# Kernel optimization log

Measured on AMD Instinct MI355X. Metric: run time of the kernel, lower is better.

The kernel has to match this reference:

```python
import jax, jax.numpy as jnp
import numpy as np

INPUT_DIM, HID, LAT, FUT = 32, 128, 64, 128
B, T = 1024, 512


def _linear(x, W, b):
    return x @ W.T + b


def _lstm_layer(xs, Wih, Whh, b):
    # xs: [T, B, D_in] -> ys: [T, B, HID], h_T: [B, HID]
    Bsz = xs.shape[1]
    h0 = jnp.zeros((Bsz, HID), xs.dtype)
    c0 = jnp.zeros((Bsz, HID), xs.dtype)

    def step(carry, xt):
        h, c = carry
        g = xt @ Wih.T + h @ Whh.T + b  # [B, 4*HID]
        i, f, gg, o = jnp.split(g, 4, axis=-1)  # torch gate order i,f,g,o
        i = jax.nn.sigmoid(i)
        f = jax.nn.sigmoid(f)
        gg = jnp.tanh(gg)
        o = jax.nn.sigmoid(o)
        c = f * c + i * gg
        h = o * jnp.tanh(c)
        return (h, c), h

    (hT, _), ys = jax.lax.scan(step, (h0, c0), xs)
    return ys, hT


def setup_inputs() -> dict:
    key = jax.random.key(0)
    ks = iter(jax.random.split(key, 40))

    def w(shape, scale=0.05):
        return (jax.random.normal(next(ks), shape, dtype=jnp.float32) * scale)

    inp = {
        "x": jax.random.normal(next(ks), (B, T, INPUT_DIM), dtype=jnp.float32),
        "eps": jax.random.normal(next(ks), (B, LAT), dtype=jnp.float32),
        "u": jax.random.uniform(next(ks), (B, LAT), dtype=jnp.float32, minval=1e-4, maxval=1 - 1e-4),
        "choice": jax.random.uniform(next(ks), (B,), dtype=jnp.float32),
        # 3-layer LSTM params (torch: W_ih [4H, D], W_hh [4H, H], fused bias)
        "Wih0": w((4 * HID, INPUT_DIM)), "Whh0": w((4 * HID, HID)), "b0": w((4 * HID,)),
        "Wih1": w((4 * HID, HID)), "Whh1": w((4 * HID, HID)), "b1": w((4 * HID,)),
        "Wih2": w((4 * HID, HID)), "Whh2": w((4 * HID, HID)), "b2": w((4 * HID,)),
        "ln_g": jnp.ones((HID,), jnp.float32), "ln_b": jnp.zeros((HID,), jnp.float32),
        "fc1_W": w((128, HID)), "fc1_b": w((128,)),
        "fc2_W": w((64, 128)), "fc2_b": w((64,)),
        "mean_W": w((LAT, 64)), "mean_b": w((LAT,)),
        "logvar_W": w((LAT, 64)), "logvar_b": w((LAT,)),
        "scale_W": w((LAT, 64)), "scale_b": w((LAT,)),
        "shape_W": w((LAT, 64)), "shape_b": w((LAT,)),
        "dec1_W": w((128, LAT)), "dec1_b": w((128,)),
        "dec2_W": w((500, 128)), "dec2_b": w((500,)),
        "out_W": w((FUT, 500)), "out_b": w((FUT,)),
        "pi_params": jnp.array([3.0, 0.01], jnp.float32),
    }
    return inp


def reference(x, eps, u, choice,
              Wih0, Whh0, b0, Wih1, Whh1, b1, Wih2, Whh2, b2,
              ln_g, ln_b, fc1_W, fc1_b, fc2_W, fc2_b,
              mean_W, mean_b, logvar_W, logvar_b,
              scale_W, scale_b, shape_W, shape_b,
              dec1_W, dec1_b, dec2_W, dec2_b, out_W, out_b, pi_params):
    # --- Encoder ---
    xs = jnp.transpose(x, (1, 0, 2))  # [T, B, D]
    ys, _ = _lstm_layer(xs, Wih0, Whh0, b0)
    ys, _ = _lstm_layer(ys, Wih1, Whh1, b1)
    _, h = _lstm_layer(ys, Wih2, Whh2, b2)  # final hidden of last layer [B, HID]
    mu = h.mean(-1, keepdims=True)
    var = jnp.mean((h - mu) ** 2, -1, keepdims=True)
    h = (h - mu) * jax.lax.rsqrt(var + 1e-5) * ln_g + ln_b
    hid = jax.nn.relu(_linear(h, fc1_W, fc1_b))
    hid = jax.nn.relu(_linear(hid, fc2_W, fc2_b))  # dropout = identity (eval)
    z_mean = _linear(hid, mean_W, mean_b)
    z_logvar = _linear(hid, logvar_W, logvar_b)
    z_scale = jnp.exp(_linear(hid, scale_W, scale_b))
    z_shape = jnp.maximum(_linear(hid, shape_W, shape_b), 1e-6)
    # --- Reparameterize (vectorized mixture select) ---
    z_gauss = z_mean + eps * jnp.exp(0.5 * z_logvar)
    z_gpd = z_scale / z_shape * ((1.0 - u) ** (-z_shape) - 1.0)
    pi = jax.nn.softmax(pi_params)
    z = jnp.where((choice < pi[0])[:, None], z_gauss, z_gpd)
    # --- Decoder ---
    d = jax.nn.relu(_linear(z, dec1_W, dec1_b))
    d = jax.nn.relu(_linear(d, dec2_W, dec2_b))  # dropout = identity (eval)
    rec = _linear(d, out_W, out_b)
    return rec, z_mean, z_logvar, z_scale, z_shape
```

## Files before the change

### kernel.cpp

```cpp
#include <hip/hip_runtime.h>
#include <math.h>

typedef __attribute__((ext_vector_type(8))) short s16x8;
typedef __attribute__((ext_vector_type(4))) float f32x4;

__device__ __forceinline__ unsigned short f2bf(float f) {
  unsigned int x = __builtin_bit_cast(unsigned int, f);
  x += 0x7fffu + ((x >> 16) & 1u);
  return (unsigned short)(x >> 16);
}
__device__ __forceinline__ float fexp2(float x) { return __builtin_amdgcn_exp2f(x); }
__device__ __forceinline__ float frcp(float x)  { return __builtin_amdgcn_rcpf(x); }
__device__ __forceinline__ float sigm(float x)  { return frcp(1.0f + fexp2(x * -1.4426950408889634f)); }
__device__ __forceinline__ float tanh_fast(float x) {
  return 1.0f - 2.0f * frcp(1.0f + fexp2(x * 2.8853900817779268f));
}

#define MFMA16(A, B, C) __builtin_amdgcn_mfma_f32_16x16x32_bf16((A), (B), (C), 0, 0, 0)

constexpr int TT = 512;
constexpr int NB = 1024;
constexpr int CHUNK = 8;

template <int DIN, bool FIRST, bool LAST>
__device__ __forceinline__ void scan_layer(
    unsigned short* a_lds,
    const float* __restrict__ xin,
    unsigned short* ys,
    const float* __restrict__ Wih,
    const float* __restrict__ Whh,
    const float* __restrict__ bias,
    float* __restrict__ hT,
    int* prog_in, int* prog_out, int bblk)
{
  constexpr int KT = DIN / 32 + 4;
  constexpr int KS = (DIN == 32) ? 192 : 256;

  const int tid = threadIdx.x;
  const int wv = tid >> 6, ln = tid & 63, l15 = ln & 15, lg = ln >> 4;
  const int row0 = bblk * 16;

  s16x8 bfr[4][KT];
#pragma unroll
  for (int j = 0; j < 4; ++j) {
    const int n = j * 128 + wv * 16 + l15;
#pragma unroll
    for (int kt = 0; kt < KT; ++kt) {
      s16x8 f;
#pragma unroll
      for (int e = 0; e < 8; ++e) {
        const int k = kt * 32 + lg * 8 + e;
        const float w = (k < DIN) ? Wih[n * DIN + k] : Whh[n * 128 + (k - DIN)];
        f[e] = (short)f2bf(w);
      }
      bfr[j][kt] = f;
    }
  }
  f32x4 bj[4];
#pragma unroll
  for (int j = 0; j < 4; ++j)
    bj[j] = *reinterpret_cast<const f32x4*>(bias + j * 128 + wv * 16 + lg * 4);

  for (int i = tid; i < 2 * 16 * KS; i += 512) a_lds[i] = 0;
  __syncthreads();

  const int prow = tid >> 5, pcol = tid & 31;
  float xr_f = 0.f;
  unsigned long long xr_h = 0ull;
  int avail = 0;

  if (FIRST) {
    xr_f = xin[(size_t)(row0 + prow) * (TT * 32) + pcol];
    a_lds[(prow * KS + pcol) ^ ((prow & 7) << 3)] = f2bf(xr_f);
  } else {
    int ch;
    do { ch = __hip_atomic_load(prog_in, __ATOMIC_RELAXED, __HIP_MEMORY_SCOPE_AGENT); } while (ch * CHUNK < 1);
    avail = ch * CHUNK;
    asm volatile("" ::: "memory");
    xr_h = __hip_atomic_load(
        (unsigned long long*)ys + ((size_t)(row0 + prow) * 128 + pcol * 4) / 4,
        __ATOMIC_RELAXED, __HIP_MEMORY_SCOPE_AGENT);
    *reinterpret_cast<unsigned long long*>(
        &a_lds[(prow * KS + pcol * 4) ^ ((prow & 7) << 3)]) = xr_h;
  }

  float cst[4] = {0.f, 0.f, 0.f, 0.f};
  const int hcol = wv * 16 + lg * 4;

  for (int t = 0; t < TT; ++t) {
    unsigned short* buf  = a_lds + (t & 1) * (16 * KS);
    unsigned short* nbuf = a_lds + ((t + 1) & 1) * (16 * KS);
    __syncthreads();

    s16x8 afr[KT];
#pragma unroll
    for (int kt = 0; kt < KT; ++kt) {
      const int idx = l15 * KS + kt * 32 + lg * 8;
      afr[kt] = *reinterpret_cast<const s16x8*>(&buf[idx ^ ((l15 & 7) << 3)]);
    }
    f32x4 acc[4];
#pragma unroll
    for (int j = 0; j < 4; ++j) acc[j] = bj[j];
#pragma unroll
    for (int kt = 0; kt < KT; ++kt)
#pragma unroll
      for (int j = 0; j < 4; ++j) acc[j] = MFMA16(bfr[j][kt], afr[kt], acc[j]);

    if (t + 1 < TT) {
      if (FIRST) {
        xr_f = xin[(size_t)(row0 + prow) * (TT * 32) + (t + 1) * 32 + pcol];
      } else {
        if (avail < t + 2) {
          int ch;
          do { ch = __hip_atomic_load(prog_in, __ATOMIC_RELAXED, __HIP_MEMORY_SCOPE_AGENT); } while (ch * CHUNK < t + 2);
          avail = ch * CHUNK;
          asm volatile("" ::: "memory");
        }
        xr_h = __hip_atomic_load(
            (unsigned long long*)ys + ((size_t)(t + 1) * (NB * 128) + (size_t)(row0 + prow) * 128 + pcol * 4) / 4,
            __ATOMIC_RELAXED, __HIP_MEMORY_SCOPE_AGENT);
      }
    }

    float hv[4];
#pragma unroll
    for (int r = 0; r < 4; ++r) {
      const float iv = sigm(acc[0][r]);
      const float fv = sigm(acc[1][r]);
      const float gv = tanh_fast(acc[2][r]);
      const float ov = sigm(acc[3][r]);
      const float cn = fv * cst[r] + iv * gv;
      cst[r] = cn;
      hv[r] = ov * tanh_fast(cn);
    }
    const unsigned int plo = (unsigned int)f2bf(hv[0]) | ((unsigned int)f2bf(hv[1]) << 16);
    const unsigned int phi = (unsigned int)f2bf(hv[2]) | ((unsigned int)f2bf(hv[3]) << 16);
    const unsigned long long hpack = (unsigned long long)plo | ((unsigned long long)phi << 32);

    *reinterpret_cast<unsigned long long*>(
        &nbuf[(l15 * KS + DIN + hcol) ^ ((l15 & 7) << 3)]) = hpack;
    if (t + 1 < TT) {
      if (FIRST) {
        nbuf[(prow * KS + pcol) ^ ((prow & 7) << 3)] = f2bf(xr_f);
      } else {
        *reinterpret_cast<unsigned long long*>(
            &nbuf[(prow * KS + pcol * 4) ^ ((prow & 7) << 3)]) = xr_h;
      }
    }

    if (!LAST) {
      __hip_atomic_store(
          (unsigned long long*)ys + ((size_t)t * (NB * 128) + (size_t)(row0 + l15) * 128 + hcol) / 4,
          hpack, __ATOMIC_RELAXED, __HIP_MEMORY_SCOPE_AGENT);
      if (((t + 1) & (CHUNK - 1)) == 0) {
        asm volatile("s_waitcnt vmcnt(0)" ::: "memory");
        __syncthreads();
        if (tid == 0)
          __hip_atomic_store(prog_out, (t + 1) / CHUNK, __ATOMIC_RELAXED, __HIP_MEMORY_SCOPE_AGENT);
      }
    } else if (t == TT - 1) {
      f32x4 o = {hv[0], hv[1], hv[2], hv[3]};
      *reinterpret_cast<f32x4*>(&hT[(row0 + l15) * 128 + hcol]) = o;
    }
  }
}

__global__ __launch_bounds__(512, 2) void lstm_fused(
    const float* __restrict__ x, unsigned short* ys,
    const float* __restrict__ Wih0, const float* __restrict__ Whh0, const float* __restrict__ b0,
    const float* __restrict__ Wih1, const float* __restrict__ Whh1, const float* __restrict__ b1,
    const float* __restrict__ Wih2, const float* __restrict__ Whh2, const float* __restrict__ b2,
    float* __restrict__ hT, int* prog)
{
  __shared__ unsigned short a_lds[2 * 16 * 256];
  const int lay = blockIdx.x >> 6;
  const int bblk = blockIdx.x & 63;
  if (lay == 0) {
    scan_layer<32, true, false>(a_lds, x, ys, Wih0, Whh0, b0, nullptr,
                                nullptr, &prog[(0 * 64 + bblk) * 4], bblk);
  } else if (lay == 1) {
    scan_layer<128, false, false>(a_lds, nullptr, ys, Wih1, Whh1, b1, nullptr,
                                  &prog[(0 * 64 + bblk) * 4], &prog[(1 * 64 + bblk) * 4], bblk);
  } else {
    scan_layer<128, false, true>(a_lds, nullptr, ys, Wih2, Whh2, b2, hT,
                                 &prog[(1 * 64 + bblk) * 4], nullptr, bblk);
  }
}

__global__ void init_flags(int* prog) { prog[threadIdx.x] = 0; }

__global__ __launch_bounds__(256) void head_kernel(
    const float* __restrict__ hT, const float* __restrict__ eps,
    const float* __restrict__ u, const float* __restrict__ choice,
    const float* __restrict__ ln_g, const float* __restrict__ ln_b,
    const float* __restrict__ fc1_W, const float* __restrict__ fc1_b,
    const float* __restrict__ fc2_W, const float* __restrict__ fc2_b,
    const float* __restrict__ mean_W, const float* __restrict__ mean_b,
    const float* __restrict__ logvar_W, const float* __restrict__ logvar_b,
    const float* __restrict__ scale_W, const float* __restrict__ scale_b,
    const float* __restrict__ shape_W, const float* __restrict__ shape_b,
    const float* __restrict__ dec1_W, const float* __restrict__ dec1_b,
    const float* __restrict__ dec2_W, const float* __restrict__ dec2_b,
    const float* __restrict__ out_W, const float* __restrict__ out_b,
    const float* __restrict__ pi_params, float* __restrict__ out)
{
  __shared__ float s_hn[4][128];
  __shared__ float s_a[4][128];
  __shared__ float s_b2[4][64];
  __shared__ float s_z[4][64];
  __shared__ float s_d1[4][128];
  __shared__ float s_d2[4][512];

  const int tid = threadIdx.x;
  const int gr0 = blockIdx.x * 4;

  {
    const int wvr = tid >> 6, lnn = tid & 63;
    const float v0 = hT[(gr0 + wvr) * 128 + lnn];
    const float v1 = hT[(gr0 + wvr) * 128 + 64 + lnn];
    float s = v0 + v1, s2 = v0 * v0 + v1 * v1;
#pragma unroll
    for (int off = 32; off; off >>= 1) {
      s  += __shfl_xor(s, off, 64);
      s2 += __shfl_xor(s2, off, 64);
    }
    const float mu  = s * (1.f / 128.f);
    const float var = s2 * (1.f / 128.f) - mu * mu;
    const float rs  = rsqrtf(var + 1e-5f);
    s_hn[wvr][lnn]      = (v0 - mu) * rs * ln_g[lnn]      + ln_b[lnn];
    s_hn[wvr][lnn + 64] = (v1 - mu) * rs * ln_g[lnn + 64] + ln_b[lnn + 64];
  }
  __syncthreads();
#pragma unroll
  for (int p = 0; p < 2; ++p) {
    const int idx = tid + p * 256, row = idx >> 7, col = idx & 127;
    const float* w = fc1_W + col * 128;
    float a = fc1_b[col];
    for (int k = 0; k < 128; k += 4)
      a += s_hn[row][k] * w[k] + s_hn[row][k + 1] * w[k + 1] +
           s_hn[row][k + 2] * w[k + 2] + s_hn[row][k + 3] * w[k + 3];
    s_a[row][col] = fmaxf(a, 0.f);
  }
  __syncthreads();
  {
    const int row = tid >> 6, col = tid & 63;
    const float* w = fc2_W + col * 128;
    float a = fc2_b[col];
    for (int k = 0; k < 128; ++k) a += s_a[row][k] * w[k];
    s_b2[row][col] = fmaxf(a, 0.f);
  }
  __syncthreads();
  {
    const int row = tid >> 6, c = tid & 63;
    const int gr = gr0 + row;
    float am = mean_b[c], al = logvar_b[c], as_ = scale_b[c], ah = shape_b[c];
    for (int k = 0; k < 64; ++k) {
      const float hv = s_b2[row][k];
      am  += hv * mean_W[c * 64 + k];
      al  += hv * logvar_W[c * 64 + k];
      as_ += hv * scale_W[c * 64 + k];
      ah  += hv * shape_W[c * 64 + k];
    }
    const float zsc = fexp2(as_ * 1.4426950408889634f);
    const float zsh = fmaxf(ah, 1e-6f);
    out[131072 + gr * 64 + c] = am;
    out[196608 + gr * 64 + c] = al;
    out[262144 + gr * 64 + c] = zsc;
    out[327680 + gr * 64 + c] = zsh;
    const float ev = eps[gr * 64 + c], uv = u[gr * 64 + c], cv = choice[gr];
    const float zg = am + ev * fexp2(0.72134752044448170f * al);
    const float p0 = pi_params[0], p1 = pi_params[1];
    const float pi0 = 1.f / (1.f + expf(p1 - p0));
    const float tq = -zsh * logf(1.f - uv);
    const float zp = zsc * frcp(zsh) * expm1f(tq);
    s_z[row][c] = (cv < pi0) ? zg : zp;
  }
  __syncthreads();
#pragma unroll
  for (int p = 0; p < 2; ++p) {
    const int idx = tid + p * 256, row = idx >> 7, col = idx & 127;
    const float* w = dec1_W + col * 64;
    float a = dec1_b[col];
    for (int k = 0; k < 64; ++k) a += s_z[row][k] * w[k];
    s_d1[row][col] = fmaxf(a, 0.f);
  }
  __syncthreads();
  for (int o = tid; o < 2000; o += 256) {
    const int row = o / 500, col = o % 500;
    const float* w = dec2_W + col * 128;
    float a = dec2_b[col];
    for (int k = 0; k < 128; ++k) a += s_d1[row][k] * w[k];
    s_d2[row][col] = fmaxf(a, 0.f);
  }
  __syncthreads();
#pragma unroll
  for (int p = 0; p < 2; ++p) {
    const int idx = tid + p * 256, row = idx >> 7, col = idx & 127;
    const float* w = out_W + col * 500;
    float a = out_b[col];
    for (int k = 0; k < 500; ++k) a += s_d2[row][k] * w[k];
    out[(gr0 + row) * 128 + col] = a;
  }
}

extern "C" void kernel_launch(void* const* d_in, const int* in_sizes, int n_in,
                              void* d_out, int out_size, void* d_ws, size_t ws_size,
                              hipStream_t stream) {
  const float* x      = (const float*)d_in[0];
  const float* eps    = (const float*)d_in[1];
  const float* u      = (const float*)d_in[2];
  const float* choice = (const float*)d_in[3];
  const float* Wih0 = (const float*)d_in[4],  *Whh0 = (const float*)d_in[5],  *b0 = (const float*)d_in[6];
  const float* Wih1 = (const float*)d_in[7],  *Whh1 = (const float*)d_in[8],  *b1 = (const float*)d_in[9];
  const float* Wih2 = (const float*)d_in[10], *Whh2 = (const float*)d_in[11], *b2 = (const float*)d_in[12];
  const float* ln_g = (const float*)d_in[13], *ln_b = (const float*)d_in[14];
  const float* fc1_W = (const float*)d_in[15], *fc1_b = (const float*)d_in[16];
  const float* fc2_W = (const float*)d_in[17], *fc2_b = (const float*)d_in[18];
  const float* mean_W = (const float*)d_in[19], *mean_b = (const float*)d_in[20];
  const float* logvar_W = (const float*)d_in[21], *logvar_b = (const float*)d_in[22];
  const float* scale_W = (const float*)d_in[23], *scale_b = (const float*)d_in[24];
  const float* shape_W = (const float*)d_in[25], *shape_b = (const float*)d_in[26];
  const float* dec1_W = (const float*)d_in[27], *dec1_b = (const float*)d_in[28];
  const float* dec2_W = (const float*)d_in[29], *dec2_b = (const float*)d_in[30];
  const float* out_W = (const float*)d_in[31], *out_b = (const float*)d_in[32];
  const float* pi_params = (const float*)d_in[33];

  unsigned short* ys = (unsigned short*)d_ws;
  float* hT  = (float*)((char*)d_ws + (size_t)512 * 1024 * 128 * 2);
  int*   prog = (int*)((char*)d_ws + (size_t)512 * 1024 * 128 * 2 + (size_t)1024 * 128 * 4);

  init_flags<<<1, 512, 0, stream>>>(prog);
  lstm_fused<<<192, 512, 0, stream>>>(x, ys, Wih0, Whh0, b0, Wih1, Whh1, b1,
                                      Wih2, Whh2, b2, hT, prog);
  head_kernel<<<256, 256, 0, stream>>>(hT, eps, u, choice, ln_g, ln_b,
      fc1_W, fc1_b, fc2_W, fc2_b, mean_W, mean_b, logvar_W, logvar_b,
      scale_W, scale_b, shape_W, shape_b, dec1_W, dec1_b, dec2_W, dec2_b,
      out_W, out_b, pi_params, (float*)d_out);
}
```

Before: 687.8 us.

## Split input projection from recurrence and batch two timesteps per sync

```diff
diff --git a/kernel.cpp b/kernel.cpp
--- a/kernel.cpp
+++ b/kernel.cpp
@@ -3,6 +3,9 @@
 
 typedef __attribute__((ext_vector_type(8))) short s16x8;
 typedef __attribute__((ext_vector_type(4))) float f32x4;
+typedef unsigned long long ull;
+
+constexpr float LOG2E = 1.4426950408889634f;
 
 __device__ __forceinline__ unsigned short f2bf(float f) {
   unsigned int x = __builtin_bit_cast(unsigned int, f);
@@ -11,156 +14,180 @@
 }
 __device__ __forceinline__ float fexp2(float x) { return __builtin_amdgcn_exp2f(x); }
 __device__ __forceinline__ float frcp(float x)  { return __builtin_amdgcn_rcpf(x); }
-__device__ __forceinline__ float sigm(float x)  { return frcp(1.0f + fexp2(x * -1.4426950408889634f)); }
-__device__ __forceinline__ float tanh_fast(float x) {
-  return 1.0f - 2.0f * frcp(1.0f + fexp2(x * 2.8853900817779268f));
-}
-
-#define MFMA16(A, B, C) __builtin_amdgcn_mfma_f32_16x16x32_bf16((A), (B), (C), 0, 0, 0)
+
+#define MFMA16(A, B, Cc) __builtin_amdgcn_mfma_f32_16x16x32_bf16((A), (B), (Cc), 0, 0, 0)
 
 constexpr int TT = 512;
 constexpr int NB = 1024;
-constexpr int CHUNK = 8;
+constexpr int CH  = 2;
+constexpr int PUB = 4;
 
 template <int DIN, bool FIRST, bool LAST>
 __device__ __forceinline__ void scan_layer(
-    unsigned short* a_lds,
+    unsigned short* x_s,
+    unsigned short* h_s,
+    float* b_s,
     const float* __restrict__ xin,
     unsigned short* ys,
-    const float* __restrict__ Wih,
-    const float* __restrict__ Whh,
-    const float* __restrict__ bias,
-    float* __restrict__ hT,
+    const float* __restrict__ Wih, const float* __restrict__ Whh,
+    const float* __restrict__ bias, float* __restrict__ hT,
     int* prog_in, int* prog_out, int bblk)
 {
-  constexpr int KT = DIN / 32 + 4;
-  constexpr int KS = (DIN == 32) ? 192 : 256;
-
+  constexpr int KTX = DIN / 32;
+  constexpr int XM  = (DIN == 32) ? 3 : 7;
   const int tid = threadIdx.x;
   const int wv = tid >> 6, ln = tid & 63, l15 = ln & 15, lg = ln >> 4;
   const int row0 = bblk * 16;
-
-  s16x8 bfr[4][KT];
+  const int prow = tid >> 5, pcol = tid & 31;
+
+  s16x8 bfx[4][KTX], bfh[4][4];
 #pragma unroll
   for (int j = 0; j < 4; ++j) {
+    const float sc = (j == 2) ? (2.0f * LOG2E) : (-LOG2E);
     const int n = j * 128 + wv * 16 + l15;
 #pragma unroll
-    for (int kt = 0; kt < KT; ++kt) {
+    for (int kt = 0; kt < KTX; ++kt) {
       s16x8 f;
 #pragma unroll
-      for (int e = 0; e < 8; ++e) {
-        const int k = kt * 32 + lg * 8 + e;
-        const float w = (k < DIN) ? Wih[n * DIN + k] : Whh[n * 128 + (k - DIN)];
-        f[e] = (short)f2bf(w);
-      }
-      bfr[j][kt] = f;
-    }
-  }
-  f32x4 bj[4];
-#pragma unroll
-  for (int j = 0; j < 4; ++j)
-    bj[j] = *reinterpret_cast<const f32x4*>(bias + j * 128 + wv * 16 + lg * 4);
-
-  for (int i = tid; i < 2 * 16 * KS; i += 512) a_lds[i] = 0;
-  __syncthreads();
-
-  const int prow = tid >> 5, pcol = tid & 31;
-  float xr_f = 0.f;
-  unsigned long long xr_h = 0ull;
+      for (int e = 0; e < 8; ++e) f[e] = (short)f2bf(Wih[n * DIN + kt * 32 + lg * 8 + e] * sc);
+      bfx[j][kt] = f;
+    }
+#pragma unroll
+    for (int kt = 0; kt < 4; ++kt) {
+      s16x8 f;
+#pragma unroll
+      for (int e = 0; e < 8; ++e) f[e] = (short)f2bf(Whh[n * 128 + kt * 32 + lg * 8 + e] * sc);
+      bfh[j][kt] = f;
+    }
+  }
+  b_s[tid] = bias[tid] * ((tid >> 7) == 2 ? 2.0f * LOG2E : -LOG2E);
+  for (int i = tid; i < 2 * 16 * 128; i += 512) h_s[i] = 0;
+
+  float xrf[CH];
+  ull xrh[CH];
   int avail = 0;
-
   if (FIRST) {
-    xr_f = xin[(size_t)(row0 + prow) * (TT * 32) + pcol];
-    a_lds[(prow * KS + pcol) ^ ((prow & 7) << 3)] = f2bf(xr_f);
+#pragma unroll
+    for (int s = 0; s < CH; ++s)
+      xrf[s] = xin[(size_t)(row0 + prow) * (TT * 32) + s * 32 + pcol];
   } else {
     int ch;
-    do { ch = __hip_atomic_load(prog_in, __ATOMIC_RELAXED, __HIP_MEMORY_SCOPE_AGENT); } while (ch * CHUNK < 1);
-    avail = ch * CHUNK;
-    asm volatile("" ::: "memory");
-    xr_h = __hip_atomic_load(
-        (unsigned long long*)ys + ((size_t)(row0 + prow) * 128 + pcol * 4) / 4,
-        __ATOMIC_RELAXED, __HIP_MEMORY_SCOPE_AGENT);
-    *reinterpret_cast<unsigned long long*>(
-        &a_lds[(prow * KS + pcol * 4) ^ ((prow & 7) << 3)]) = xr_h;
-  }
+    do { ch = __hip_atomic_load(prog_in, __ATOMIC_RELAXED, __HIP_MEMORY_SCOPE_AGENT); } while (ch * PUB < CH);
+    avail = ch * PUB;
+#pragma unroll
+    for (int s = 0; s < CH; ++s)
+      xrh[s] = __hip_atomic_load(
+          (ull*)ys + ((size_t)s * (NB * 128) + (size_t)(row0 + prow) * 128 + pcol * 4) / 4,
+          __ATOMIC_RELAXED, __HIP_MEMORY_SCOPE_AGENT);
+  }
+  __syncthreads();
 
   float cst[4] = {0.f, 0.f, 0.f, 0.f};
   const int hcol = wv * 16 + lg * 4;
 
-  for (int t = 0; t < TT; ++t) {
-    unsigned short* buf  = a_lds + (t & 1) * (16 * KS);
-    unsigned short* nbuf = a_lds + ((t + 1) & 1) * (16 * KS);
+  for (int t0 = 0; t0 < TT; t0 += CH) {
+    if (FIRST) {
+#pragma unroll
+      for (int s = 0; s < CH; ++s)
+        x_s[s * (16 * DIN) + prow * DIN + (pcol ^ ((prow & XM) << 3))] = f2bf(xrf[s]);
+    } else {
+#pragma unroll
+      for (int s = 0; s < CH; ++s)
+        *reinterpret_cast<ull*>(
+            &x_s[s * (16 * DIN) + prow * DIN + ((pcol * 4) ^ ((prow & 7) << 3))]) = xrh[s];
+    }
     __syncthreads();
 
-    s16x8 afr[KT];
-#pragma unroll
-    for (int kt = 0; kt < KT; ++kt) {
-      const int idx = l15 * KS + kt * 32 + lg * 8;
-      afr[kt] = *reinterpret_cast<const s16x8*>(&buf[idx ^ ((l15 & 7) << 3)]);
-    }
-    f32x4 acc[4];
-#pragma unroll
-    for (int j = 0; j < 4; ++j) acc[j] = bj[j];
-#pragma unroll
-    for (int kt = 0; kt < KT; ++kt)
-#pragma unroll
-      for (int j = 0; j < 4; ++j) acc[j] = MFMA16(bfr[j][kt], afr[kt], acc[j]);
-
-    if (t + 1 < TT) {
+    f32x4 gx[CH][4];
+#pragma unroll
+    for (int s = 0; s < CH; ++s) {
+#pragma unroll
+      for (int j = 0; j < 4; ++j)
+        gx[s][j] = *reinterpret_cast<const f32x4*>(&b_s[j * 128 + wv * 16 + lg * 4]);
+#pragma unroll
+      for (int kt = 0; kt < KTX; ++kt) {
+        const s16x8 xf = *reinterpret_cast<const s16x8*>(
+            &x_s[s * (16 * DIN) + l15 * DIN + ((kt * 32 + lg * 8) ^ ((l15 & XM) << 3))]);
+#pragma unroll
+        for (int j = 0; j < 4; ++j) gx[s][j] = MFMA16(bfx[j][kt], xf, gx[s][j]);
+      }
+    }
+
+    const int t1 = t0 + CH;
+    if (t1 < TT) {
       if (FIRST) {
-        xr_f = xin[(size_t)(row0 + prow) * (TT * 32) + (t + 1) * 32 + pcol];
+#pragma unroll
+        for (int s = 0; s < CH; ++s)
+          xrf[s] = xin[(size_t)(row0 + prow) * (TT * 32) + (t1 + s) * 32 + pcol];
       } else {
-        if (avail < t + 2) {
+        if (avail < t1 + CH) {
           int ch;
-          do { ch = __hip_atomic_load(prog_in, __ATOMIC_RELAXED, __HIP_MEMORY_SCOPE_AGENT); } while (ch * CHUNK < t + 2);
-          avail = ch * CHUNK;
-          asm volatile("" ::: "memory");
+          do { ch = __hip_atomic_load(prog_in, __ATOMIC_RELAXED, __HIP_MEMORY_SCOPE_AGENT); } while (ch * PUB < t1 + CH);
+          avail = ch * PUB;
         }
-        xr_h = __hip_atomic_load(
-            (unsigned long long*)ys + ((size_t)(t + 1) * (NB * 128) + (size_t)(row0 + prow) * 128 + pcol * 4) / 4,
-            __ATOMIC_RELAXED, __HIP_MEMORY_SCOPE_AGENT);
+#pragma unroll
+        for (int s = 0; s < CH; ++s)
+          xrh[s] = __hip_atomic_load(
+              (ull*)ys + ((size_t)(t1 + s) * (NB * 128) + (size_t)(row0 + prow) * 128 + pcol * 4) / 4,
+              __ATOMIC_RELAXED, __HIP_MEMORY_SCOPE_AGENT);
       }
     }
 
-    float hv[4];
-#pragma unroll
-    for (int r = 0; r < 4; ++r) {
-      const float iv = sigm(acc[0][r]);
-      const float fv = sigm(acc[1][r]);
-      const float gv = tanh_fast(acc[2][r]);
-      const float ov = sigm(acc[3][r]);
-      const float cn = fv * cst[r] + iv * gv;
-      cst[r] = cn;
-      hv[r] = ov * tanh_fast(cn);
-    }
-    const unsigned int plo = (unsigned int)f2bf(hv[0]) | ((unsigned int)f2bf(hv[1]) << 16);
-    const unsigned int phi = (unsigned int)f2bf(hv[2]) | ((unsigned int)f2bf(hv[3]) << 16);
-    const unsigned long long hpack = (unsigned long long)plo | ((unsigned long long)phi << 32);
-
-    *reinterpret_cast<unsigned long long*>(
-        &nbuf[(l15 * KS + DIN + hcol) ^ ((l15 & 7) << 3)]) = hpack;
-    if (t + 1 < TT) {
-      if (FIRST) {
-        nbuf[(prow * KS + pcol) ^ ((prow & 7) << 3)] = f2bf(xr_f);
-      } else {
-        *reinterpret_cast<unsigned long long*>(
-            &nbuf[(prow * KS + pcol * 4) ^ ((prow & 7) << 3)]) = xr_h;
+#pragma unroll
+    for (int s = 0; s < CH; ++s) {
+      const int t = t0 + s;
+      if (s) __syncthreads();
+      unsigned short* buf  = h_s + (t & 1) * (16 * 128);
+      unsigned short* nbuf = h_s + ((t + 1) & 1) * (16 * 128);
+      s16x8 afr[4];
+#pragma unroll
+      for (int kt = 0; kt < 4; ++kt)
+        afr[kt] = *reinterpret_cast<const s16x8*>(
+            &buf[l15 * 128 + ((kt * 32 + lg * 8) ^ ((l15 & 7) << 3))]);
+      f32x4 acc[4];
+#pragma unroll
+      for (int j = 0; j < 4; ++j) acc[j] = gx[s][j];
+#pragma unroll
+      for (int kt = 0; kt < 4; ++kt)
+#pragma unroll
+        for (int j = 0; j < 4; ++j) acc[j] = MFMA16(bfh[j][kt], afr[kt], acc[j]);
+
+      float hv[4];
+#pragma unroll
+      for (int r = 0; r < 4; ++r) {
+        const float iv = frcp(1.0f + fexp2(acc[0][r]));
+        const float fv = frcp(1.0f + fexp2(acc[1][r]));
+        const float gv = 1.0f - 2.0f * frcp(1.0f + fexp2(acc[2][r]));
+        const float ov = frcp(1.0f + fexp2(acc[3][r]));
+        const float cn = fv * cst[r] + iv * gv;
+        cst[r] = cn;
+        const float th = 1.0f - 2.0f * frcp(1.0f + fexp2(cn * (2.0f * LOG2E)));
+        hv[r] = ov * th;
       }
-    }
-
-    if (!LAST) {
-      __hip_atomic_store(
-          (unsigned long long*)ys + ((size_t)t * (NB * 128) + (size_t)(row0 + l15) * 128 + hcol) / 4,
-          hpack, __ATOMIC_RELAXED, __HIP_MEMORY_SCOPE_AGENT);
-      if (((t + 1) & (CHUNK - 1)) == 0) {
-        asm volatile("s_waitcnt vmcnt(0)" ::: "memory");
-        __syncthreads();
-        if (tid == 0)
-          __hip_atomic_store(prog_out, (t + 1) / CHUNK, __ATOMIC_RELAXED, __HIP_MEMORY_SCOPE_AGENT);
+      unsigned int plo, phi;
+      asm("v_cvt_pk_bf16_f32 %0, %1, %2" : "=v"(plo) : "v"(hv[0]), "v"(hv[1]));
+      asm("v_cvt_pk_bf16_f32 %0, %1, %2" : "=v"(phi) : "v"(hv[2]), "v"(hv[3]));
+      const ull hpack = (ull)plo | ((ull)phi << 32);
+
+      *reinterpret_cast<ull*>(&nbuf[l15 * 128 + (hcol ^ ((l15 & 7) << 3))]) = hpack;
+
+      if (!LAST) {
+        __hip_atomic_store(
+            (ull*)ys + ((size_t)t * (NB * 128) + (size_t)(row0 + l15) * 128 + hcol) / 4,
+            hpack, __ATOMIC_RELAXED, __HIP_MEMORY_SCOPE_AGENT);
+      } else if (t == TT - 1) {
+        f32x4 o = {hv[0], hv[1], hv[2], hv[3]};
+        *reinterpret_cast<f32x4*>(&hT[(row0 + l15) * 128 + hcol]) = o;
       }
-    } else if (t == TT - 1) {
-      f32x4 o = {hv[0], hv[1], hv[2], hv[3]};
-      *reinterpret_cast<f32x4*>(&hT[(row0 + l15) * 128 + hcol]) = o;
+    }
+
+    if (!LAST && ((t0 + CH) % PUB) == 0) {
+      asm volatile("s_waitcnt vmcnt(0)" ::: "memory");
+      __syncthreads();
+      if (tid == 0)
+        __hip_atomic_store(prog_out, (t0 + CH) / PUB, __ATOMIC_RELAXED, __HIP_MEMORY_SCOPE_AGENT);
+    } else {
+      __syncthreads();
     }
   }
 }
@@ -172,22 +199,27 @@
     const float* __restrict__ Wih2, const float* __restrict__ Whh2, const float* __restrict__ b2,
     float* __restrict__ hT, int* prog)
 {
-  __shared__ unsigned short a_lds[2 * 16 * 256];
+  __shared__ unsigned short x_s[CH * 16 * 128];
+  __shared__ unsigned short h_s[2 * 16 * 128];
+  __shared__ float b_s[512];
   const int lay = blockIdx.x >> 6;
   const int bblk = blockIdx.x & 63;
   if (lay == 0) {
-    scan_layer<32, true, false>(a_lds, x, ys, Wih0, Whh0, b0, nullptr,
-                                nullptr, &prog[(0 * 64 + bblk) * 4], bblk);
+    scan_layer<32, true, false>(x_s, h_s, b_s, x, ys, Wih0, Whh0, b0, nullptr,
+                                nullptr, &prog[(0 * 64 + bblk) * 16], bblk);
   } else if (lay == 1) {
-    scan_layer<128, false, false>(a_lds, nullptr, ys, Wih1, Whh1, b1, nullptr,
-                                  &prog[(0 * 64 + bblk) * 4], &prog[(1 * 64 + bblk) * 4], bblk);
+    scan_layer<128, false, false>(x_s, h_s, b_s, nullptr, ys, Wih1, Whh1, b1, nullptr,
+                                  &prog[(0 * 64 + bblk) * 16], &prog[(1 * 64 + bblk) * 16], bblk);
   } else {
-    scan_layer<128, false, true>(a_lds, nullptr, ys, Wih2, Whh2, b2, hT,
-                                 &prog[(1 * 64 + bblk) * 4], nullptr, bblk);
-  }
-}
-
-__global__ void init_flags(int* prog) { prog[threadIdx.x] = 0; }
+    scan_layer<128, false, true>(x_s, h_s, b_s, nullptr, ys, Wih2, Whh2, b2, hT,
+                                 &prog[(1 * 64 + bblk) * 16], nullptr, bblk);
+  }
+}
+
+__global__ void init_flags(int* prog) {
+  prog[threadIdx.x] = 0;
+  prog[threadIdx.x + 1024] = 0;
+}
 
 __global__ __launch_bounds__(256) void head_kernel(
     const float* __restrict__ hT, const float* __restrict__ eps,
@@ -261,7 +293,7 @@
       as_ += hv * scale_W[c * 64 + k];
       ah  += hv * shape_W[c * 64 + k];
     }
-    const float zsc = fexp2(as_ * 1.4426950408889634f);
+    const float zsc = fexp2(as_ * LOG2E);
     const float zsh = fmaxf(ah, 1e-6f);
     out[131072 + gr * 64 + c] = am;
     out[196608 + gr * 64 + c] = al;
@@ -329,7 +361,7 @@
   float* hT  = (float*)((char*)d_ws + (size_t)512 * 1024 * 128 * 2);
   int*   prog = (int*)((char*)d_ws + (size_t)512 * 1024 * 128 * 2 + (size_t)1024 * 128 * 4);
 
-  init_flags<<<1, 512, 0, stream>>>(prog);
+  init_flags<<<1, 1024, 0, stream>>>(prog);
   lstm_fused<<<192, 512, 0, stream>>>(x, ys, Wih0, Whh0, b0, Wih1, Whh1, b1,
                                       Wih2, Whh2, b2, hT, prog);
   head_kernel<<<256, 256, 0, stream>>>(hT, eps, u, choice, ln_g, ln_b,
```

Result: no change. 676.9 us (-1.6%).
